# Performance work log

Hardware: AMD Instinct MI355X
Metric: run time of the kernel (lower is better)

Reference implementation:

```python
import jax, jax.numpy as jnp
import numpy as np

B, S, D, H = 1, 2048, 4096, 32
NEG = -1e9  # stands in for jnp.NINF in the source; finite to avoid NaNs in fully-masked rows


def _rope_tables(seq_len, dim):
    # cos/sin tables spanning the FULL hidden dim (RoPE here is applied pre-head-split)
    inv_freq = 1.0 / (10000.0 ** (np.arange(0, dim // 2, dtype=np.float32) / (dim // 2)))
    t = np.arange(seq_len, dtype=np.float32)
    freqs = np.outer(t, inv_freq)            # (S, D/2)
    emb = np.concatenate([freqs, freqs], -1)  # (S, D)
    return np.cos(emb)[None], np.sin(emb)[None]  # (1, S, D)


def setup_inputs() -> dict:
    key = jax.random.key(0)
    ks = jax.random.split(key, 5)
    cos, sin = _rope_tables(S, D)
    return {
        "hidden_state": jax.random.normal(ks[0], (B, S, D), jnp.float32),
        "attn_mask": jnp.zeros((B, 1, S, S), jnp.float32),
        "cos": jnp.asarray(cos),
        "sin": jnp.asarray(sin),
        "wq": jax.random.normal(ks[1], (D, D), jnp.float32) * 0.02,
        "wk": jax.random.normal(ks[2], (D, D), jnp.float32) * 0.02,
        "wv": jax.random.normal(ks[3], (D, D), jnp.float32) * 0.02,
        "wo": jax.random.normal(ks[4], (D, D), jnp.float32) * 0.02,
    }


def _rotate_half(x):
    x1, x2 = x[..., : x.shape[-1] // 2], x[..., x.shape[-1] // 2 :]
    return jnp.concatenate((-x2, x1), axis=-1)


def reference(hidden_state, attn_mask, cos, sin, wq, wk, wv, wo):
    b, s, d = hidden_state.shape
    h, hd = H, d // H
    # QKV projections (no bias), RoPE applied over the full hidden dim (pre-split, as in source)
    q = hidden_state @ wq
    k = hidden_state @ wk
    v = hidden_state @ wv
    q = q * cos + _rotate_half(q) * sin
    k = k * cos + _rotate_half(k) * sin
    split = lambda x: jnp.transpose(x.reshape(b, s, h, hd), (0, 2, 1, 3))  # (b,h,s,hd)
    q, k, v = split(q), split(k), split(v)
    # NOTE: source scales by sqrt(full hidden d), not sqrt(head_dim)
    scores = jnp.einsum("bhqd,bhkd->bhqk", q, k) / jnp.sqrt(jnp.float32(d))
    # source masks the LOWER triangle (incl. diagonal); replicated faithfully with finite NEG
    tri = jnp.tri(s, s, dtype=jnp.float32)
    mask = jnp.where(tri == 1, NEG, 0.0)[None, None]  # (1,1,s,s)
    scores = scores + attn_mask + mask
    attn = jax.nn.softmax(scores, axis=-1)
    out = jnp.einsum("bhqk,bhkd->bhqd", attn, v)
    out = jnp.transpose(out, (0, 2, 1, 3)).reshape(b, s, d)
    return out @ wo
```

## Files before the change

kernel.cpp:

```cpp
#include <hip/hip_runtime.h>
#include <stdint.h>


#define SS 2048
#define DD 4096
#define NH 32
#define HD 128
#define NEGV -1000000000.0f
#define LDP 136

typedef __bf16 bf16x8 __attribute__((ext_vector_type(8)));
typedef float f32x4 __attribute__((ext_vector_type(4)));

__device__ __forceinline__ float bf2f(uint16_t u) {
    union { uint32_t i; float f; } v; v.i = ((uint32_t)u) << 16; return v.f;
}
__device__ __forceinline__ uint16_t f2bf(float f) {
    union { float f; uint32_t i; } v; v.f = f;
    uint32_t x = v.i;
    uint32_t r = (x + 0x7fffu + ((x >> 16) & 1u)) >> 16;
    return (uint16_t)r;
}

__device__ __forceinline__ void storeOut(float* C, size_t i, float v) { C[i] = v; }
__device__ __forceinline__ void storeOut(uint16_t* C, size_t i, float v) { C[i] = f2bf(v); }

__global__ void xconv_kernel(const float* __restrict__ in, uint16_t* __restrict__ out) {
    int i = blockIdx.x * blockDim.x + threadIdx.x;
    const float4* in4 = (const float4*)in;
    float4 a = in4[2 * i], b = in4[2 * i + 1];
    uint4 o;
    o.x = (uint32_t)f2bf(a.x) | ((uint32_t)f2bf(a.y) << 16);
    o.y = (uint32_t)f2bf(a.z) | ((uint32_t)f2bf(a.w) << 16);
    o.z = (uint32_t)f2bf(b.x) | ((uint32_t)f2bf(b.y) << 16);
    o.w = (uint32_t)f2bf(b.z) | ((uint32_t)f2bf(b.w) << 16);
    ((uint4*)out)[i] = o;
}

__global__ void wtrans_kernel(const float* __restrict__ in,
                              uint16_t* __restrict__ out) {
    __shared__ uint16_t tile[32][33];
    int bx = blockIdx.x * 32, by = blockIdx.y * 32;
    int tx = threadIdx.x, ty = threadIdx.y;
    #pragma unroll
    for (int i = 0; i < 32; i += 8)
        tile[ty + i][tx] = f2bf(in[(size_t)(by + ty + i) * DD + bx + tx]);
    __syncthreads();
    #pragma unroll
    for (int i = 0; i < 32; i += 8)
        out[(size_t)(bx + ty + i) * DD + by + tx] = tile[tx][ty + i];
}

template <typename OutT>
__global__ __launch_bounds__(256) void gemm_bt(const uint16_t* __restrict__ A,
                                               const uint16_t* __restrict__ Bt,
                                               OutT* __restrict__ C,
                                               int M, int N, int K) {
    __shared__ uint16_t sA[128 * 32];
    __shared__ uint16_t sB[128 * 32];
    int t = threadIdx.x;
    int lane = t & 63, w = t >> 6;
    int wm = (w >> 1) * 64, wn = (w & 1) * 64;
    int rowBase = blockIdx.y * 128, colBase = blockIdx.x * 128;
    f32x4 acc[4][4] = {};

    int lr = lane & 15;
    int kq = (lane >> 4) * 8;

    for (int k0 = 0; k0 < K; k0 += 32) {
        __syncthreads();
        #pragma unroll
        for (int p = 0; p < 2; ++p) {
            int c = p * 256 + t;
            int r = c >> 2;
            int cc = (c & 3) * 8;
            *(uint4*)(&sA[r * 32 + cc]) =
                *(const uint4*)(&A[(size_t)(rowBase + r) * K + k0 + cc]);
            *(uint4*)(&sB[r * 32 + cc]) =
                *(const uint4*)(&Bt[(size_t)(colBase + r) * K + k0 + cc]);
        }
        __syncthreads();

        bf16x8 af[4], bfr[4];
        #pragma unroll
        for (int i = 0; i < 4; ++i) {
            af[i]  = *(const bf16x8*)(&sA[(wm + i * 16 + lr) * 32 + kq]);
            bfr[i] = *(const bf16x8*)(&sB[(wn + i * 16 + lr) * 32 + kq]);
        }
        #pragma unroll
        for (int mt = 0; mt < 4; ++mt)
            #pragma unroll
            for (int nt = 0; nt < 4; ++nt)
                acc[mt][nt] = __builtin_amdgcn_mfma_f32_16x16x32_bf16(
                    af[mt], bfr[nt], acc[mt][nt], 0, 0, 0);
    }

    int q = lane >> 4;
    #pragma unroll
    for (int mt = 0; mt < 4; ++mt)
        #pragma unroll
        for (int nt = 0; nt < 4; ++nt)
            #pragma unroll
            for (int r = 0; r < 4; ++r) {
                int row = rowBase + wm + mt * 16 + q * 4 + r;
                int col = colBase + wn + nt * 16 + lr;
                storeOut(C, (size_t)row * N + col, acc[mt][nt][r]);
            }
}

__global__ void rope_kernel(uint16_t* __restrict__ q, uint16_t* __restrict__ k,
                            const float* __restrict__ cosb,
                            const float* __restrict__ sinb) {
    int idx = blockIdx.x * blockDim.x + threadIdx.x;
    int s = idx >> 11;
    int d = idx & 2047;
    size_t i0 = (size_t)s * DD + d, i1 = i0 + 2048;
    float c0 = cosb[i0], c1 = cosb[i1];
    float s0 = sinb[i0], s1 = sinb[i1];
    float q0 = bf2f(q[i0]), q1 = bf2f(q[i1]);
    q[i0] = f2bf(q0 * c0 - q1 * s0);
    q[i1] = f2bf(q1 * c1 + q0 * s1);
    float k0 = bf2f(k[i0]), k1 = bf2f(k[i1]);
    k[i0] = f2bf(k0 * c0 - k1 * s0);
    k[i1] = f2bf(k1 * c1 + k0 * s1);
}

__global__ __launch_bounds__(256) void fattn_kernel(
    const uint16_t* __restrict__ Q, const uint16_t* __restrict__ K,
    const uint16_t* __restrict__ VT, const float* __restrict__ mask,
    uint16_t* __restrict__ O)
{
    __shared__ uint16_t sQ[64 * LDP];
    __shared__ uint16_t sK[128 * LDP];
    __shared__ uint16_t sVt[128 * LDP];
    __shared__ uint16_t sP[64 * LDP];
    __shared__ float sAlpha[64];
    __shared__ float sL[64];

    int h = blockIdx.y, q0 = blockIdx.x * 64;
    int base = h * HD;
    int t = threadIdx.x;
    int lane = t & 63, w = t >> 6;
    int lr = lane & 15, quad = lane >> 4;
    int mw = w * 16;

    for (int c = t; c < 64 * 16; c += 256) {
        int m = c >> 4, dc = (c & 15) * 8;
        *(uint4*)(&sQ[m * LDP + dc]) =
            *(const uint4*)(&Q[(size_t)(q0 + m) * DD + base + dc]);
    }

    f32x4 oacc[2][4] = {};
    float m_pr[4], l_run[4];
    #pragma unroll
    for (int r = 0; r < 4; ++r) { m_pr[r] = -3.0e38f; l_run[r] = 0.f; }

    for (int kt = 0; kt < SS / 128; ++kt) {
        __syncthreads();
        for (int c = t; c < 128 * 16; c += 256) {
            int r = c >> 4, dc = (c & 15) * 8;
            *(uint4*)(&sK[r * LDP + dc]) =
                *(const uint4*)(&K[(size_t)(kt * 128 + r) * DD + base + dc]);
            *(uint4*)(&sVt[r * LDP + dc]) =
                *(const uint4*)(&VT[(size_t)(base + r) * SS + kt * 128 + dc]);
        }
        __syncthreads();

        f32x4 sacc[8] = {};
        #pragma unroll
        for (int kc = 0; kc < 4; ++kc) {
            bf16x8 af = *(const bf16x8*)(&sQ[(mw + lr) * LDP + kc * 32 + quad * 8]);
            #pragma unroll
            for (int nt = 0; nt < 8; ++nt) {
                bf16x8 bfr = *(const bf16x8*)(&sK[(nt * 16 + lr) * LDP + kc * 32 + quad * 8]);
                sacc[nt] = __builtin_amdgcn_mfma_f32_16x16x32_bf16(af, bfr, sacc[nt], 0, 0, 0);
            }
        }

        float sc[8][4];
        #pragma unroll
        for (int nt = 0; nt < 8; ++nt) {
            int kk = kt * 128 + nt * 16 + lr;
            #pragma unroll
            for (int r = 0; r < 4; ++r) {
                int qrow = q0 + mw + quad * 4 + r;
                float s = sacc[nt][r] * 0.015625f + mask[(size_t)qrow * SS + kk];
                if (kk <= qrow) s += NEGV;
                sc[nt][r] = s;
            }
        }

        float mnew[4], alpha[4];
        #pragma unroll
        for (int r = 0; r < 4; ++r) {
            float mx = sc[0][r];
            #pragma unroll
            for (int nt = 1; nt < 8; ++nt) mx = fmaxf(mx, sc[nt][r]);
            #pragma unroll
            for (int off = 1; off < 16; off <<= 1)
                mx = fmaxf(mx, __shfl_xor(mx, off));
            mnew[r] = fmaxf(m_pr[r], mx);
            alpha[r] = __expf(m_pr[r] - mnew[r]);
            m_pr[r] = mnew[r];
        }

        float ps[4] = {0.f, 0.f, 0.f, 0.f};
        #pragma unroll
        for (int nt = 0; nt < 8; ++nt) {
            #pragma unroll
            for (int r = 0; r < 4; ++r) {
                float p = __expf(sc[nt][r] - mnew[r]);
                ps[r] += p;
                sP[(mw + quad * 4 + r) * LDP + nt * 16 + lr] = f2bf(p);
            }
        }
        #pragma unroll
        for (int r = 0; r < 4; ++r) {
            #pragma unroll
            for (int off = 1; off < 16; off <<= 1)
                ps[r] += __shfl_xor(ps[r], off);
            l_run[r] = l_run[r] * alpha[r] + ps[r];
            if (lr == 0) sAlpha[mw + quad * 4 + r] = alpha[r];
        }
        __syncthreads();

        float a_col[4];
        #pragma unroll
        for (int nt = 0; nt < 4; ++nt) a_col[nt] = sAlpha[nt * 16 + lr];
        #pragma unroll
        for (int dt = 0; dt < 2; ++dt)
            #pragma unroll
            for (int nt = 0; nt < 4; ++nt)
                #pragma unroll
                for (int r = 0; r < 4; ++r)
                    oacc[dt][nt][r] *= a_col[nt];
        #pragma unroll
        for (int kc = 0; kc < 4; ++kc) {
            bf16x8 bfr[4];
            #pragma unroll
            for (int nt = 0; nt < 4; ++nt)
                bfr[nt] = *(const bf16x8*)(&sP[(nt * 16 + lr) * LDP + kc * 32 + quad * 8]);
            #pragma unroll
            for (int dt = 0; dt < 2; ++dt) {
                bf16x8 af = *(const bf16x8*)(&sVt[((2 * w + dt) * 16 + lr) * LDP + kc * 32 + quad * 8]);
                #pragma unroll
                for (int nt = 0; nt < 4; ++nt)
                    oacc[dt][nt] = __builtin_amdgcn_mfma_f32_16x16x32_bf16(af, bfr[nt], oacc[dt][nt], 0, 0, 0);
            }
        }
    }

    #pragma unroll
    for (int r = 0; r < 4; ++r)
        if (lr == 0) sL[mw + quad * 4 + r] = l_run[r];
    __syncthreads();

    float linv[4];
    #pragma unroll
    for (int nt = 0; nt < 4; ++nt) linv[nt] = 1.f / sL[nt * 16 + lr];
    #pragma unroll
    for (int dt = 0; dt < 2; ++dt) {
        int ddl = (2 * w + dt) * 16 + quad * 4;
        #pragma unroll
        for (int nt = 0; nt < 4; ++nt) {
            int ml = nt * 16 + lr;
            #pragma unroll
            for (int r = 0; r < 4; ++r)
                sK[ml * LDP + ddl + r] = f2bf(oacc[dt][nt][r] * linv[nt]);
        }
    }
    __syncthreads();
    for (int c = t; c < 64 * 16; c += 256) {
        int m = c >> 4, dc = (c & 15) * 8;
        *(uint4*)(&O[(size_t)(q0 + m) * DD + base + dc]) =
            *(const uint4*)(&sK[m * LDP + dc]);
    }
}

extern "C" void kernel_launch(void* const* d_in, const int* in_sizes, int n_in,
                              void* d_out, int out_size, void* d_ws, size_t ws_size,
                              hipStream_t stream) {
    const float* X    = (const float*)d_in[0];
    const float* mask = (const float*)d_in[1];
    const float* cosb = (const float*)d_in[2];
    const float* sinb = (const float*)d_in[3];
    const float* wq   = (const float*)d_in[4];
    const float* wk   = (const float*)d_in[5];
    const float* wv   = (const float*)d_in[6];
    const float* wo   = (const float*)d_in[7];
    float* out = (float*)d_out;

    char* ws = (char*)d_ws;
    uint16_t* Wt  = (uint16_t*)ws;
    uint16_t* Xbf = (uint16_t*)(ws + (size_t)33554432);
    uint16_t* Q   = Xbf + (size_t)SS * DD;
    uint16_t* Kb  = Q  + (size_t)SS * DD;
    uint16_t* VT  = Kb + (size_t)SS * DD;
    uint16_t* AO  = Xbf;

    dim3 tgrid(DD / 32, DD / 32), tblock(32, 8);
    dim3 ggrid(DD / 128, SS / 128), gblock(256);

    xconv_kernel<<<(SS * DD) / (256 * 8), 256, 0, stream>>>(X, Xbf);

    wtrans_kernel<<<tgrid, tblock, 0, stream>>>(wq, Wt);
    gemm_bt<<<ggrid, gblock, 0, stream>>>(Xbf, Wt, Q, SS, DD, DD);
    wtrans_kernel<<<tgrid, tblock, 0, stream>>>(wk, Wt);
    gemm_bt<<<ggrid, gblock, 0, stream>>>(Xbf, Wt, Kb, SS, DD, DD);
    wtrans_kernel<<<tgrid, tblock, 0, stream>>>(wv, Wt);
    gemm_bt<<<dim3(SS / 128, DD / 128), gblock, 0, stream>>>(Wt, Xbf, VT, DD, SS, DD);

    rope_kernel<<<(SS * 2048) / 256, 256, 0, stream>>>(Q, Kb, cosb, sinb);

    fattn_kernel<<<dim3(SS / 64, NH), 256, 0, stream>>>(Q, Kb, VT, mask, AO);

    wtrans_kernel<<<tgrid, tblock, 0, stream>>>(wo, Wt);
    gemm_bt<<<ggrid, gblock, 0, stream>>>(AO, Wt, out, SS, DD, DD);
}
```

Baseline: 1.183 ms.

## Skip fully-masked key tiles, shrink attention tiles, use global_load_lds in GEMM

The attention kernel now uses 64-key tiles and starts its key loop at the query block's tile index, skipping tiles the lower-triangle mask fully kills. The last query block keeps the full range so its fully-masked rows still come out as a uniform softmax. The GEMM stages tiles straight from global memory into LDS with global_load_lds, and s_setprio raises wave priority around the MFMA sections. Smaller tiles mean more loop iterations and more syncs per key.

New measurement: 1.111 ms. 6.1% less time.

```diff
diff --git a/kernel.cpp b/kernel.cpp
--- a/kernel.cpp
+++ b/kernel.cpp
@@ -8,9 +8,15 @@
 #define HD 128
 #define NEGV -1000000000.0f
 #define LDP 136
+#define LDV 72
 
 typedef __bf16 bf16x8 __attribute__((ext_vector_type(8)));
 typedef float f32x4 __attribute__((ext_vector_type(4)));
+
+#define GLDS16(gp, lp)                                                        \
+    __builtin_amdgcn_global_load_lds(                                         \
+        (__attribute__((address_space(1))) uint32_t*)(uintptr_t)(gp),         \
+        (__attribute__((address_space(3))) uint32_t*)(uintptr_t)(lp), 16, 0, 0)
 
 __device__ __forceinline__ float bf2f(uint16_t u) {
     union { uint32_t i; float f; } v; v.i = ((uint32_t)u) << 16; return v.f;
@@ -56,8 +62,8 @@
                                                const uint16_t* __restrict__ Bt,
                                                OutT* __restrict__ C,
                                                int M, int N, int K) {
-    __shared__ uint16_t sA[128 * 32];
-    __shared__ uint16_t sB[128 * 32];
+    __shared__ __attribute__((aligned(16))) uint16_t sA[128 * 32];
+    __shared__ __attribute__((aligned(16))) uint16_t sB[128 * 32];
     int t = threadIdx.x;
     int lane = t & 63, w = t >> 6;
     int wm = (w >> 1) * 64, wn = (w & 1) * 64;
@@ -74,10 +80,8 @@
             int c = p * 256 + t;
             int r = c >> 2;
             int cc = (c & 3) * 8;
-            *(uint4*)(&sA[r * 32 + cc]) =
-                *(const uint4*)(&A[(size_t)(rowBase + r) * K + k0 + cc]);
-            *(uint4*)(&sB[r * 32 + cc]) =
-                *(const uint4*)(&Bt[(size_t)(colBase + r) * K + k0 + cc]);
+            GLDS16(&A[(size_t)(rowBase + r) * K + k0 + cc], &sA[c * 8]);
+            GLDS16(&Bt[(size_t)(colBase + r) * K + k0 + cc], &sB[c * 8]);
         }
         __syncthreads();
 
@@ -130,10 +134,10 @@
     const uint16_t* __restrict__ VT, const float* __restrict__ mask,
     uint16_t* __restrict__ O)
 {
-    __shared__ uint16_t sQ[64 * LDP];
-    __shared__ uint16_t sK[128 * LDP];
-    __shared__ uint16_t sVt[128 * LDP];
-    __shared__ uint16_t sP[64 * LDP];
+    __shared__ __attribute__((aligned(16))) uint16_t sQ[64 * LDP];
+    __shared__ __attribute__((aligned(16))) uint16_t sK[64 * LDP];
+    __shared__ __attribute__((aligned(16))) uint16_t sVt[HD * LDV];
+    __shared__ __attribute__((aligned(16))) uint16_t sP[64 * LDV];
     __shared__ float sAlpha[64];
     __shared__ float sL[64];
 
@@ -155,32 +159,38 @@
     #pragma unroll
     for (int r = 0; r < 4; ++r) { m_pr[r] = -3.0e38f; l_run[r] = 0.f; }
 
-    for (int kt = 0; kt < SS / 128; ++kt) {
-        __syncthreads();
-        for (int c = t; c < 128 * 16; c += 256) {
+    int kt_lo = (q0 == SS - 64) ? 0 : blockIdx.x;
+    for (int kt = kt_lo; kt < SS / 64; ++kt) {
+        __syncthreads();
+        for (int c = t; c < 64 * 16; c += 256) {
             int r = c >> 4, dc = (c & 15) * 8;
             *(uint4*)(&sK[r * LDP + dc]) =
-                *(const uint4*)(&K[(size_t)(kt * 128 + r) * DD + base + dc]);
-            *(uint4*)(&sVt[r * LDP + dc]) =
-                *(const uint4*)(&VT[(size_t)(base + r) * SS + kt * 128 + dc]);
-        }
-        __syncthreads();
-
-        f32x4 sacc[8] = {};
+                *(const uint4*)(&K[(size_t)(kt * 64 + r) * DD + base + dc]);
+        }
+        for (int c = t; c < 128 * 8; c += 256) {
+            int r = c >> 3, dc = (c & 7) * 8;
+            *(uint4*)(&sVt[r * LDV + dc]) =
+                *(const uint4*)(&VT[(size_t)(base + r) * SS + kt * 64 + dc]);
+        }
+        __syncthreads();
+
+        f32x4 sacc[4] = {};
+        __builtin_amdgcn_s_setprio(1);
         #pragma unroll
         for (int kc = 0; kc < 4; ++kc) {
             bf16x8 af = *(const bf16x8*)(&sQ[(mw + lr) * LDP + kc * 32 + quad * 8]);
             #pragma unroll
-            for (int nt = 0; nt < 8; ++nt) {
+            for (int nt = 0; nt < 4; ++nt) {
                 bf16x8 bfr = *(const bf16x8*)(&sK[(nt * 16 + lr) * LDP + kc * 32 + quad * 8]);
                 sacc[nt] = __builtin_amdgcn_mfma_f32_16x16x32_bf16(af, bfr, sacc[nt], 0, 0, 0);
             }
         }
-
-        float sc[8][4];
-        #pragma unroll
-        for (int nt = 0; nt < 8; ++nt) {
-            int kk = kt * 128 + nt * 16 + lr;
+        __builtin_amdgcn_s_setprio(0);
+
+        float sc[4][4];
+        #pragma unroll
+        for (int nt = 0; nt < 4; ++nt) {
+            int kk = kt * 64 + nt * 16 + lr;
             #pragma unroll
             for (int r = 0; r < 4; ++r) {
                 int qrow = q0 + mw + quad * 4 + r;
@@ -195,7 +205,7 @@
         for (int r = 0; r < 4; ++r) {
             float mx = sc[0][r];
             #pragma unroll
-            for (int nt = 1; nt < 8; ++nt) mx = fmaxf(mx, sc[nt][r]);
+            for (int nt = 1; nt < 4; ++nt) mx = fmaxf(mx, sc[nt][r]);
             #pragma unroll
             for (int off = 1; off < 16; off <<= 1)
                 mx = fmaxf(mx, __shfl_xor(mx, off));
@@ -206,12 +216,12 @@
 
         float ps[4] = {0.f, 0.f, 0.f, 0.f};
         #pragma unroll
-        for (int nt = 0; nt < 8; ++nt) {
+        for (int nt = 0; nt < 4; ++nt) {
             #pragma unroll
             for (int r = 0; r < 4; ++r) {
                 float p = __expf(sc[nt][r] - mnew[r]);
                 ps[r] += p;
-                sP[(mw + quad * 4 + r) * LDP + nt * 16 + lr] = f2bf(p);
+                sP[(mw + quad * 4 + r) * LDV + nt * 16 + lr] = f2bf(p);
             }
         }
         #pragma unroll
@@ -234,20 +244,22 @@
                 #pragma unroll
                 for (int r = 0; r < 4; ++r)
                     oacc[dt][nt][r] *= a_col[nt];
-        #pragma unroll
-        for (int kc = 0; kc < 4; ++kc) {
+        __builtin_amdgcn_s_setprio(1);
+        #pragma unroll
+        for (int kc = 0; kc < 2; ++kc) {
             bf16x8 bfr[4];
             #pragma unroll
             for (int nt = 0; nt < 4; ++nt)
-                bfr[nt] = *(const bf16x8*)(&sP[(nt * 16 + lr) * LDP + kc * 32 + quad * 8]);
+                bfr[nt] = *(const bf16x8*)(&sP[(nt * 16 + lr) * LDV + kc * 32 + quad * 8]);
             #pragma unroll
             for (int dt = 0; dt < 2; ++dt) {
-                bf16x8 af = *(const bf16x8*)(&sVt[((2 * w + dt) * 16 + lr) * LDP + kc * 32 + quad * 8]);
+                bf16x8 af = *(const bf16x8*)(&sVt[((2 * w + dt) * 16 + lr) * LDV + kc * 32 + quad * 8]);
                 #pragma unroll
                 for (int nt = 0; nt < 4; ++nt)
                     oacc[dt][nt] = __builtin_amdgcn_mfma_f32_16x16x32_bf16(af, bfr[nt], oacc[dt][nt], 0, 0, 0);
             }
         }
+        __builtin_amdgcn_s_setprio(0);
     }
 
     #pragma unroll
```
